# Performance work log

Hardware: AMD Instinct MI355X
Metric: run time of the kernel (lower is better)

## Reference

```python
import jax, jax.numpy as jnp
import numpy as np

# Sobel kernels stacked as [O=2, I=1, 3, 3]
_KX = np.array([[-1., 0., 1.], [-2., 0., 2.], [-1., 0., 1.]], dtype=np.float32)
_KY = np.array([[1., 2., 1.], [0., 0., 0.], [-1., -2., -1.]], dtype=np.float32)
_SOBEL_W = jnp.asarray(np.stack([_KX, _KY])[:, None, :, :])  # [2,1,3,3]


def _sobel(x):
    # x: [B,1,H,W] -> |Gx| + |Gy| : [B,1,H,W]
    g = jax.lax.conv_general_dilated(
        x, _SOBEL_W, window_strides=(1, 1), padding=((1, 1), (1, 1)),
        dimension_numbers=('NCHW', 'OIHW', 'NCHW'))  # [B,2,H,W]
    return jnp.sum(jnp.abs(g), axis=1, keepdims=True)


def _threshold_mask(g, k):
    # g: [B,1,H,W]; k-th SMALLEST over flattened (C*H*W) per batch (torch.kthvalue)
    B, N, H, W = g.shape
    flat = g.reshape(B, N, H * W)
    kth = jnp.sort(flat, axis=-1)[:, :, k - 1:k]  # [B,N,1]
    mask = (flat >= kth).astype(g.dtype)
    return mask.reshape(B, N, H, W)


def setup_inputs() -> dict:
    key = jax.random.key(0)
    kA, kB, kF = jax.random.split(key, 3)
    shape = (8, 3, 1024, 1024)
    return {
        'image_A': jax.random.uniform(kA, shape, dtype=jnp.float32),
        'image_B': jax.random.uniform(kB, shape, dtype=jnp.float32),
        'image_fused': jax.random.uniform(kF, shape, dtype=jnp.float32),
        'thresholds': 524288,
    }


def reference(image_A, image_B, image_fused, thresholds):
    gA = _sobel(image_A[:, :1])
    gB = _sobel(image_B[:, :1])
    gF = _sobel(image_fused[:, :1])
    joint_max = jnp.maximum(gA, gB)  # max over concat([gA,gB], dim=1) with 1 ch each
    maskA = _threshold_mask(gA, thresholds)
    maskB = _threshold_mask(gB, thresholds)
    loss = jnp.mean(jnp.abs(gF - joint_max))
    return (loss, maskA, maskB)
```

## Files before the change

### kernel.cpp

```cpp
#include <hip/hip_runtime.h>

#define IMG_H 1024
#define IMG_W 1024
#define NBATCH 8
#define NCH 3
#define NPIX (IMG_H * IMG_W)
#define SEGS 64
#define NTOT (8388608LL)

#define BINS1 4096
#define SH1 19

#define WS_MISC_OFF   0
#define WS_MISC_BYTES 4096
#define WS_H1R_OFF    (WS_MISC_OFF + WS_MISC_BYTES)
#define WS_H1R_BYTES  (2 * NBATCH * BINS1 * 4)
#define WS_H1P_OFF    (WS_H1R_OFF + WS_H1R_BYTES)
#define WS_H1P_BYTES  (2 * NBATCH * SEGS * BINS1 * 2)
#define WS_LIST_OFF   (WS_H1P_OFF + WS_H1P_BYTES)

struct Row3f { float l, c, r; };

__device__ __forceinline__ Row3f load3(const float* __restrict__ img, int y, int x) {
    Row3f o;
    if ((unsigned)y >= (unsigned)IMG_H) { o.l = o.c = o.r = 0.0f; return o; }
    const float* row = img + (size_t)y * IMG_W;
    o.c = row[x];
    o.l = (x > 0)         ? row[x - 1] : 0.0f;
    o.r = (x < IMG_W - 1) ? row[x + 1] : 0.0f;
    return o;
}

__device__ __forceinline__ float sobel_g(const Row3f& r0, const Row3f& r1, const Row3f& r2) {
    float gx = r0.r - r0.l;
    gx -= 2.0f * r1.l;
    gx += 2.0f * r1.r;
    gx -= r2.l;
    gx += r2.r;
    float gy = r0.l + 2.0f * r0.c;
    gy += r0.r;
    gy -= r2.l;
    gy -= 2.0f * r2.c;
    gy -= r2.r;
    return fabsf(gx) + fabsf(gy);
}

extern "C" __global__ __launch_bounds__(512)
void k_pass0(const float* __restrict__ A, const float* __restrict__ B,
             const float* __restrict__ F,
             unsigned short* __restrict__ hist1p, double* __restrict__ lossAcc)
{
    __shared__ unsigned int h[4 * BINS1];
    __shared__ double lsum[8];
    const int t = threadIdx.x;
    for (int i = t; i < 4 * BINS1; i += 512) h[i] = 0u;
    __syncthreads();

    const int blk = blockIdx.x;
    const int batch = blk >> 6;
    const int seg = blk & 63;
    const int y0 = (seg >> 1) * 32;
    const int x  = (seg & 1) * 512 + t;
    unsigned int* hc = h + (t >> 8) * (2 * BINS1);

    const float* a = A + (size_t)batch * NCH * NPIX;
    const float* b = B + (size_t)batch * NCH * NPIX;
    const float* f = F + (size_t)batch * NCH * NPIX;

    Row3f a0 = load3(a, y0 - 1, x), a1 = load3(a, y0, x), a2;
    Row3f b0 = load3(b, y0 - 1, x), b1 = load3(b, y0, x), b2;
    Row3f f0 = load3(f, y0 - 1, x), f1 = load3(f, y0, x), f2;

    double loss = 0.0;
    for (int i = 0; i < 32; ++i) {
        const int y = y0 + i;
        a2 = load3(a, y + 1, x);
        b2 = load3(b, y + 1, x);
        f2 = load3(f, y + 1, x);
        const float gA = sobel_g(a0, a1, a2);
        const float gB = sobel_g(b0, b1, b2);
        const float gF = sobel_g(f0, f1, f2);
        atomicAdd(&hc[__float_as_uint(gA) >> SH1], 1u);
        atomicAdd(&hc[BINS1 + (__float_as_uint(gB) >> SH1)], 1u);
        loss += (double)fabsf(gF - fmaxf(gA, gB));
        a0 = a1; a1 = a2;
        b0 = b1; b1 = b2;
        f0 = f1; f1 = f2;
    }
    __syncthreads();

    unsigned short* oA = hist1p + ((size_t)batch            * SEGS + seg) * BINS1;
    unsigned short* oB = hist1p + ((size_t)(NBATCH + batch) * SEGS + seg) * BINS1;
    for (int i = t; i < 2 * BINS1; i += 512) {
        const unsigned v = h[i] + h[2 * BINS1 + i];
        if (i < BINS1) oA[i] = (unsigned short)v;
        else           oB[i - BINS1] = (unsigned short)v;
    }

    for (int off = 32; off > 0; off >>= 1) loss += __shfl_down(loss, off);
    if ((t & 63) == 0) lsum[t >> 6] = loss;
    __syncthreads();
    if (t == 0) {
        double s = 0.0;
        for (int i = 0; i < 8; ++i) s += lsum[i];
        atomicAdd(lossAcc, s);
    }
}

extern "C" __global__ __launch_bounds__(256)
void k_scan1a(const unsigned short* __restrict__ hist1p, unsigned int* __restrict__ hist1r)
{
    const int idx = blockIdx.x * 256 + threadIdx.x;
    const int ib  = idx >> 12;
    const int bin = idx & (BINS1 - 1);
    const unsigned short* p = hist1p + (size_t)ib * SEGS * BINS1 + bin;
    unsigned int s = 0;
    #pragma unroll 8
    for (int sg = 0; sg < SEGS; ++sg) s += p[(size_t)sg * BINS1];
    hist1r[idx] = s;
}

extern "C" __global__ __launch_bounds__(1024)
void k_scan1b(const unsigned int* __restrict__ hist1r, const int* __restrict__ kptr,
              int* __restrict__ sel1, int* __restrict__ resid1)
{
    const int ib = blockIdx.x, t = threadIdx.x;
    const unsigned int* hr = hist1r + (size_t)ib * BINS1;
    long long kl = (long long)kptr[0];
    if (kl < 1 || kl > (long long)NPIX) {
        float kf = ((const float*)kptr)[0];
        kl = (long long)kf;
        if (kl < 1) kl = 1;
        if (kl > NPIX) kl = NPIX;
    }
    const unsigned k = (unsigned)kl;

    const uint4 c = ((const uint4*)hr)[t];
    const unsigned s = c.x + c.y + c.z + c.w;
    __shared__ unsigned ls[1024];
    ls[t] = s; __syncthreads();
    for (int off = 1; off < 1024; off <<= 1) {
        unsigned v = (t >= off) ? ls[t - off] : 0u;
        __syncthreads();
        ls[t] += v;
        __syncthreads();
    }
    const unsigned incl = ls[t];
    const unsigned excl = incl - s;
    if (excl < k && k <= incl) {
        unsigned cum = excl; int bin = t * 4;
        if (cum + c.x < k) { cum += c.x; ++bin;
          if (cum + c.y < k) { cum += c.y; ++bin;
            if (cum + c.z < k) { cum += c.z; ++bin; } } }
        sel1[ib] = bin;
        resid1[ib] = (int)(k - cum);
    }
}

#define PB_ROWS 32
extern "C" __global__ __launch_bounds__(1024)
void k_passB(const float* __restrict__ A, const float* __restrict__ B,
             const int* __restrict__ sel1, unsigned int* __restrict__ gCnt,
             uint2* __restrict__ list, unsigned cap, float* __restrict__ out)
{
    const int t = threadIdx.x;
    const int blk = blockIdx.x;
    const int batch = blk >> 5;
    const int y0 = (blk & 31) * PB_ROWS;
    const int x = t;

    const float* a = A + (size_t)batch * NCH * NPIX;
    const float* b = B + (size_t)batch * NCH * NPIX;
    const unsigned sA = (unsigned)sel1[batch];
    const unsigned sB = (unsigned)sel1[NBATCH + batch];
    float* mA = out + 1 + (size_t)batch * NPIX;
    float* mB = out + 1 + (size_t)NTOT + (size_t)batch * NPIX;

    __shared__ uint2 bufA[2048], bufB[2048];
    __shared__ unsigned cntA, cntB, baseA, baseB;
    if (t == 0) { cntA = 0u; cntB = 0u; }
    __syncthreads();

    Row3f a0 = load3(a, y0 - 1, x), a1 = load3(a, y0, x), a2;
    Row3f b0 = load3(b, y0 - 1, x), b1 = load3(b, y0, x), b2;
    for (int i = 0; i < PB_ROWS; ++i) {
        const int y = y0 + i;
        a2 = load3(a, y + 1, x);
        b2 = load3(b, y + 1, x);
        const unsigned uA = __float_as_uint(sobel_g(a0, a1, a2));
        const unsigned uB = __float_as_uint(sobel_g(b0, b1, b2));
        const unsigned binA = uA >> SH1, binB = uB >> SH1;
        const unsigned idx = (unsigned)y * IMG_W + (unsigned)x;
        mA[idx] = (binA > sA) ? 1.0f : 0.0f;
        mB[idx] = (binB > sB) ? 1.0f : 0.0f;
        if (binA == sA) { unsigned p = atomicAdd(&cntA, 1u); bufA[p] = make_uint2(uA, idx); }
        if (binB == sB) { unsigned p = atomicAdd(&cntB, 1u); bufB[p] = make_uint2(uB, idx); }
        a0 = a1; a1 = a2;
        b0 = b1; b1 = b2;

        __syncthreads();
        const bool last = (i == PB_ROWS - 1);
        const unsigned nA = cntA, nB = cntB;
        const bool doA = (nA >= 1024u) || (last && nA > 0u);
        const bool doB = (nB >= 1024u) || (last && nB > 0u);
        if (doA || doB) {
            if (t == 0) {
                if (doA) baseA = atomicAdd(&gCnt[batch], nA);
                if (doB) baseB = atomicAdd(&gCnt[NBATCH + batch], nB);
            }
            __syncthreads();
            if (doA) {
                const unsigned bs = baseA;
                for (unsigned j = t; j < nA; j += 1024u) {
                    const unsigned d = bs + j;
                    if (d < cap) list[(size_t)batch * cap + d] = bufA[j];
                }
            }
            if (doB) {
                const unsigned bs = baseB;
                for (unsigned j = t; j < nB; j += 1024u) {
                    const unsigned d = bs + j;
                    if (d < cap) list[(size_t)(NBATCH + batch) * cap + d] = bufB[j];
                }
            }
            __syncthreads();
            if (t == 0) { if (doA) cntA = 0u; if (doB) cntB = 0u; }
        }
        __syncthreads();
    }
}

extern "C" __global__ __launch_bounds__(1024)
void k_selectfix(const uint2* __restrict__ list, const unsigned int* __restrict__ gCnt,
                 unsigned cap, const int* __restrict__ sel1, const int* __restrict__ resid1,
                 const double* __restrict__ lossAcc, float* __restrict__ out)
{
    const int ib = blockIdx.x, t = threadIdx.x;
    const unsigned n = min(gCnt[ib], cap);
    const unsigned kk = (unsigned)resid1[ib];
    const uint2* L = list + (size_t)ib * cap;

    __shared__ unsigned h2[BINS1];
    __shared__ unsigned ls[1024];
    __shared__ unsigned bcast[4];
    if (t < 4) bcast[t] = 0u;
    for (int i = t; i < BINS1; i += 1024) h2[i] = 0u;
    __syncthreads();

    for (unsigned j = t; j < n; j += 1024u) atomicAdd(&h2[(L[j].x >> 7) & 4095u], 1u);
    __syncthreads();

    const unsigned c0 = h2[4 * t], c1 = h2[4 * t + 1], c2 = h2[4 * t + 2], c3 = h2[4 * t + 3];
    const unsigned s = c0 + c1 + c2 + c3;
    ls[t] = s; __syncthreads();
    for (int off = 1; off < 1024; off <<= 1) {
        unsigned v = (t >= off) ? ls[t - off] : 0u;
        __syncthreads();
        ls[t] += v;
        __syncthreads();
    }
    {
        const unsigned incl = ls[t], excl = incl - s;
        if (excl < kk && kk <= incl) {
            unsigned cum = excl; unsigned bin = 4u * t;
            if (cum + c0 < kk) { cum += c0; ++bin;
              if (cum + c1 < kk) { cum += c1; ++bin;
                if (cum + c2 < kk) { cum += c2; ++bin; } } }
            bcast[0] = bin;
            bcast[1] = kk - cum;
        }
    }
    __syncthreads();
    const unsigned sel2 = bcast[0], k3 = bcast[1];

    if (t < 128) h2[t] = 0u;
    __syncthreads();
    for (unsigned j = t; j < n; j += 1024u) {
        const unsigned b = L[j].x;
        if (((b >> 7) & 4095u) == sel2) atomicAdd(&h2[b & 127u], 1u);
    }
    __syncthreads();
    {
        const unsigned s3 = (t < 128) ? h2[t] : 0u;
        ls[t] = s3; __syncthreads();
        for (int off = 1; off < 1024; off <<= 1) {
            unsigned v = (t >= off) ? ls[t - off] : 0u;
            __syncthreads();
            ls[t] += v;
            __syncthreads();
        }
        const unsigned incl = ls[t], excl = incl - s3;
        if (t < 128 && excl < k3 && k3 <= incl) {
            bcast[2] = ((unsigned)sel1[ib] << SH1) | (sel2 << 7) | (unsigned)t;
        }
    }
    __syncthreads();
    const unsigned kth = bcast[2];

    float* m = out + 1 + (size_t)ib * NPIX;
    for (unsigned j = t; j < n; j += 1024u) {
        const uint2 e = L[j];
        m[e.y] = (e.x >= kth) ? 1.0f : 0.0f;
    }
    if (ib == 0 && t == 0) out[0] = (float)(lossAcc[0] * (1.0 / 8388608.0));
}

extern "C" void kernel_launch(void* const* d_in, const int* in_sizes, int n_in,
                              void* d_out, int out_size, void* d_ws, size_t ws_size,
                              hipStream_t stream)
{
    const float* A = (const float*)d_in[0];
    const float* B = (const float*)d_in[1];
    const float* F = (const float*)d_in[2];
    const int* kptr = (const int*)d_in[3];
    float* out = (float*)d_out;

    if (ws_size < (size_t)WS_LIST_OFF + 16 * 8 * 1024) return;

    char* ws = (char*)d_ws;
    double* lossAcc        = (double*)(ws + WS_MISC_OFF);
    unsigned int* gCnt     = (unsigned int*)(ws + WS_MISC_OFF + 64);
    unsigned int* hist1r   = (unsigned int*)(ws + WS_H1R_OFF);
    unsigned short* hist1p = (unsigned short*)(ws + WS_H1P_OFF);
    uint2* list            = (uint2*)(ws + WS_LIST_OFF);
    int* sel1              = (int*)(ws + WS_MISC_OFF + 128);
    int* resid1            = (int*)(ws + WS_MISC_OFF + 256);

    unsigned long long capll = (ws_size - WS_LIST_OFF) / (16ull * 8ull);
    unsigned cap = (capll > (unsigned long long)NPIX) ? (unsigned)NPIX : (unsigned)capll;

    hipMemsetAsync(ws, 0, WS_MISC_BYTES, stream);

    k_pass0    <<<dim3(NBATCH * SEGS), dim3(512), 0, stream>>>(A, B, F, hist1p, lossAcc);
    k_scan1a   <<<dim3(2 * NBATCH * BINS1 / 256), dim3(256), 0, stream>>>(hist1p, hist1r);
    k_scan1b   <<<dim3(2 * NBATCH), dim3(1024), 0, stream>>>(hist1r, kptr, sel1, resid1);
    k_passB    <<<dim3(NBATCH * 32), dim3(1024), 0, stream>>>(A, B, sel1, gCnt, list, cap, out);
    k_selectfix<<<dim3(2 * NBATCH), dim3(1024), 0, stream>>>(list, gCnt, cap, sel1, resid1, lossAcc, out);
}
```

Before: 346.9 us.

## Merge histogram via global atomics, drop scan kernel, use wave-shuffle scans

Per-block histograms are now added directly into the global reduced histogram with atomics on nonzero bins. This removes the 16-bit partial-histogram buffer and the separate reduction kernel. The loss is written as per-block partials and summed inside the new select kernel, which also resets the list counters so the misc memset can go. Block-wide prefix scans are replaced by wave shuffle scans plus a small cross-wave pass, cutting barrier count. Pass0 and passB now use 1024 threads with 16-row segments, doubling passB's grid, at the cost of global atomic contention on the shared histogram.

Measured after the change: 322.5 us. -7.0%, faster.

```diff
diff --git a/kernel.cpp b/kernel.cpp
--- a/kernel.cpp
+++ b/kernel.cpp
@@ -5,19 +5,20 @@
 #define NBATCH 8
 #define NCH 3
 #define NPIX (IMG_H * IMG_W)
-#define SEGS 64
 #define NTOT (8388608LL)
 
 #define BINS1 4096
 #define SH1 19
 
+#define SEGS 64
+#define ROWS_PER_SEG 16
+
 #define WS_MISC_OFF   0
-#define WS_MISC_BYTES 4096
-#define WS_H1R_OFF    (WS_MISC_OFF + WS_MISC_BYTES)
+#define WS_H1R_OFF    4096
 #define WS_H1R_BYTES  (2 * NBATCH * BINS1 * 4)
-#define WS_H1P_OFF    (WS_H1R_OFF + WS_H1R_BYTES)
-#define WS_H1P_BYTES  (2 * NBATCH * SEGS * BINS1 * 2)
-#define WS_LIST_OFF   (WS_H1P_OFF + WS_H1P_BYTES)
+#define WS_LOSSP_OFF  (WS_H1R_OFF + WS_H1R_BYTES)
+#define WS_LOSSP_BYTES (NBATCH * SEGS * 8)
+#define WS_LIST_OFF   (WS_LOSSP_OFF + WS_LOSSP_BYTES)
 
 struct Row3f { float l, c, r; };
 
@@ -45,23 +46,32 @@
     return fabsf(gx) + fabsf(gy);
 }
 
-extern "C" __global__ __launch_bounds__(512)
+__device__ __forceinline__ unsigned wave_scan(unsigned s, int lane) {
+    #pragma unroll
+    for (int off = 1; off < 64; off <<= 1) {
+        const unsigned v = __shfl_up(s, off);
+        if (lane >= off) s += v;
+    }
+    return s;
+}
+
+extern "C" __global__ __launch_bounds__(1024)
 void k_pass0(const float* __restrict__ A, const float* __restrict__ B,
              const float* __restrict__ F,
-             unsigned short* __restrict__ hist1p, double* __restrict__ lossAcc)
+             unsigned int* __restrict__ hist1r, double* __restrict__ lossPart)
 {
     __shared__ unsigned int h[4 * BINS1];
-    __shared__ double lsum[8];
+    __shared__ double lsum[16];
     const int t = threadIdx.x;
-    for (int i = t; i < 4 * BINS1; i += 512) h[i] = 0u;
+    const int lane = t & 63;
+    for (int i = t; i < 4 * BINS1; i += 1024) h[i] = 0u;
     __syncthreads();
 
     const int blk = blockIdx.x;
     const int batch = blk >> 6;
-    const int seg = blk & 63;
-    const int y0 = (seg >> 1) * 32;
-    const int x  = (seg & 1) * 512 + t;
-    unsigned int* hc = h + (t >> 8) * (2 * BINS1);
+    const int y0 = (blk & 63) * ROWS_PER_SEG;
+    const int x = t;
+    unsigned int* hc = h + (t >> 9) * (2 * BINS1);
 
     const float* a = A + (size_t)batch * NCH * NPIX;
     const float* b = B + (size_t)batch * NCH * NPIX;
@@ -72,7 +82,7 @@
     Row3f f0 = load3(f, y0 - 1, x), f1 = load3(f, y0, x), f2;
 
     double loss = 0.0;
-    for (int i = 0; i < 32; ++i) {
+    for (int i = 0; i < ROWS_PER_SEG; ++i) {
         const int y = y0 + i;
         a2 = load3(a, y + 1, x);
         b2 = load3(b, y + 1, x);
@@ -89,43 +99,34 @@
     }
     __syncthreads();
 
-    unsigned short* oA = hist1p + ((size_t)batch            * SEGS + seg) * BINS1;
-    unsigned short* oB = hist1p + ((size_t)(NBATCH + batch) * SEGS + seg) * BINS1;
-    for (int i = t; i < 2 * BINS1; i += 512) {
+    for (int i = t; i < 2 * BINS1; i += 1024) {
         const unsigned v = h[i] + h[2 * BINS1 + i];
-        if (i < BINS1) oA[i] = (unsigned short)v;
-        else           oB[i - BINS1] = (unsigned short)v;
+        if (v) {
+            unsigned int* dst = (i < BINS1)
+                ? &hist1r[(size_t)batch * BINS1 + i]
+                : &hist1r[(size_t)(NBATCH + batch) * BINS1 + (i - BINS1)];
+            atomicAdd(dst, v);
+        }
     }
 
     for (int off = 32; off > 0; off >>= 1) loss += __shfl_down(loss, off);
-    if ((t & 63) == 0) lsum[t >> 6] = loss;
+    if (lane == 0) lsum[t >> 6] = loss;
     __syncthreads();
     if (t == 0) {
         double s = 0.0;
-        for (int i = 0; i < 8; ++i) s += lsum[i];
-        atomicAdd(lossAcc, s);
-    }
-}
-
-extern "C" __global__ __launch_bounds__(256)
-void k_scan1a(const unsigned short* __restrict__ hist1p, unsigned int* __restrict__ hist1r)
-{
-    const int idx = blockIdx.x * 256 + threadIdx.x;
-    const int ib  = idx >> 12;
-    const int bin = idx & (BINS1 - 1);
-    const unsigned short* p = hist1p + (size_t)ib * SEGS * BINS1 + bin;
-    unsigned int s = 0;
-    #pragma unroll 8
-    for (int sg = 0; sg < SEGS; ++sg) s += p[(size_t)sg * BINS1];
-    hist1r[idx] = s;
+        for (int i = 0; i < 16; ++i) s += lsum[i];
+        lossPart[blk] = s;
+    }
 }
 
 extern "C" __global__ __launch_bounds__(1024)
-void k_scan1b(const unsigned int* __restrict__ hist1r, const int* __restrict__ kptr,
-              int* __restrict__ sel1, int* __restrict__ resid1)
+void k_select1(const unsigned int* __restrict__ hist1r, const double* __restrict__ lossPart,
+               const int* __restrict__ kptr, int* __restrict__ sel1, int* __restrict__ resid1,
+               double* __restrict__ lossAcc, unsigned int* __restrict__ gCnt)
 {
     const int ib = blockIdx.x, t = threadIdx.x;
-    const unsigned int* hr = hist1r + (size_t)ib * BINS1;
+    const int lane = t & 63, wid = t >> 6;
+
     long long kl = (long long)kptr[0];
     if (kl < 1 || kl > (long long)NPIX) {
         float kf = ((const float*)kptr)[0];
@@ -135,17 +136,22 @@
     }
     const unsigned k = (unsigned)kl;
 
-    const uint4 c = ((const uint4*)hr)[t];
+    const uint4 c = ((const uint4*)(hist1r + (size_t)ib * BINS1))[t];
     const unsigned s = c.x + c.y + c.z + c.w;
-    __shared__ unsigned ls[1024];
-    ls[t] = s; __syncthreads();
-    for (int off = 1; off < 1024; off <<= 1) {
-        unsigned v = (t >= off) ? ls[t - off] : 0u;
-        __syncthreads();
-        ls[t] += v;
-        __syncthreads();
-    }
-    const unsigned incl = ls[t];
+
+    unsigned incl = wave_scan(s, lane);
+    __shared__ unsigned wsum[16];
+    __shared__ double dsum[16];
+    if (lane == 63) wsum[wid] = incl;
+    __syncthreads();
+    if (wid == 0) {
+        unsigned w = (lane < 16) ? wsum[lane] : 0u;
+        w = wave_scan(w, lane);
+        if (lane < 16) wsum[lane] = w;
+    }
+    __syncthreads();
+    if (wid > 0) incl += wsum[wid - 1];
+
     const unsigned excl = incl - s;
     if (excl < k && k <= incl) {
         unsigned cum = excl; int bin = t * 4;
@@ -155,9 +161,20 @@
         sel1[ib] = bin;
         resid1[ib] = (int)(k - cum);
     }
-}
-
-#define PB_ROWS 32
+
+    double v = 0.0;
+    if (ib == 0 && t < NBATCH * SEGS) v = lossPart[t];
+    for (int off = 32; off > 0; off >>= 1) v += __shfl_down(v, off);
+    if (lane == 0) dsum[wid] = v;
+    __syncthreads();
+    if (ib == 0 && t == 0) {
+        double sL = 0.0;
+        for (int i = 0; i < 16; ++i) sL += dsum[i];
+        lossAcc[0] = sL;
+    }
+    if (t == 0) gCnt[ib] = 0u;
+}
+
 extern "C" __global__ __launch_bounds__(1024)
 void k_passB(const float* __restrict__ A, const float* __restrict__ B,
              const int* __restrict__ sel1, unsigned int* __restrict__ gCnt,
@@ -165,8 +182,8 @@
 {
     const int t = threadIdx.x;
     const int blk = blockIdx.x;
-    const int batch = blk >> 5;
-    const int y0 = (blk & 31) * PB_ROWS;
+    const int batch = blk >> 6;
+    const int y0 = (blk & 63) * ROWS_PER_SEG;
     const int x = t;
 
     const float* a = A + (size_t)batch * NCH * NPIX;
@@ -183,7 +200,7 @@
 
     Row3f a0 = load3(a, y0 - 1, x), a1 = load3(a, y0, x), a2;
     Row3f b0 = load3(b, y0 - 1, x), b1 = load3(b, y0, x), b2;
-    for (int i = 0; i < PB_ROWS; ++i) {
+    for (int i = 0; i < ROWS_PER_SEG; ++i) {
         const int y = y0 + i;
         a2 = load3(a, y + 1, x);
         b2 = load3(b, y + 1, x);
@@ -199,7 +216,7 @@
         b0 = b1; b1 = b2;
 
         __syncthreads();
-        const bool last = (i == PB_ROWS - 1);
+        const bool last = (i == ROWS_PER_SEG - 1);
         const unsigned nA = cntA, nB = cntB;
         const bool doA = (nA >= 1024u) || (last && nA > 0u);
         const bool doB = (nB >= 1024u) || (last && nB > 0u);
@@ -236,12 +253,13 @@
                  const double* __restrict__ lossAcc, float* __restrict__ out)
 {
     const int ib = blockIdx.x, t = threadIdx.x;
-    const unsigned n = min(gCnt[ib], cap);
+    const int lane = t & 63, wid = t >> 6;
+    unsigned n = gCnt[ib]; if (n > cap) n = cap;
     const unsigned kk = (unsigned)resid1[ib];
     const uint2* L = list + (size_t)ib * cap;
 
     __shared__ unsigned h2[BINS1];
-    __shared__ unsigned ls[1024];
+    __shared__ unsigned wsum[16];
     __shared__ unsigned bcast[4];
     if (t < 4) bcast[t] = 0u;
     for (int i = t; i < BINS1; i += 1024) h2[i] = 0u;
@@ -252,15 +270,18 @@
 
     const unsigned c0 = h2[4 * t], c1 = h2[4 * t + 1], c2 = h2[4 * t + 2], c3 = h2[4 * t + 3];
     const unsigned s = c0 + c1 + c2 + c3;
-    ls[t] = s; __syncthreads();
-    for (int off = 1; off < 1024; off <<= 1) {
-        unsigned v = (t >= off) ? ls[t - off] : 0u;
-        __syncthreads();
-        ls[t] += v;
-        __syncthreads();
-    }
+    unsigned incl = wave_scan(s, lane);
+    if (lane == 63) wsum[wid] = incl;
+    __syncthreads();
+    if (wid == 0) {
+        unsigned w = (lane < 16) ? wsum[lane] : 0u;
+        w = wave_scan(w, lane);
+        if (lane < 16) wsum[lane] = w;
+    }
+    __syncthreads();
+    if (wid > 0) incl += wsum[wid - 1];
     {
-        const unsigned incl = ls[t], excl = incl - s;
+        const unsigned excl = incl - s;
         if (excl < kk && kk <= incl) {
             unsigned cum = excl; unsigned bin = 4u * t;
             if (cum + c0 < kk) { cum += c0; ++bin;
@@ -276,21 +297,24 @@
     if (t < 128) h2[t] = 0u;
     __syncthreads();
     for (unsigned j = t; j < n; j += 1024u) {
-        const unsigned b = L[j].x;
-        if (((b >> 7) & 4095u) == sel2) atomicAdd(&h2[b & 127u], 1u);
+        const unsigned bbits = L[j].x;
+        if (((bbits >> 7) & 4095u) == sel2) atomicAdd(&h2[bbits & 127u], 1u);
     }
     __syncthreads();
     {
         const unsigned s3 = (t < 128) ? h2[t] : 0u;
-        ls[t] = s3; __syncthreads();
-        for (int off = 1; off < 1024; off <<= 1) {
-            unsigned v = (t >= off) ? ls[t - off] : 0u;
-            __syncthreads();
-            ls[t] += v;
-            __syncthreads();
-        }
-        const unsigned incl = ls[t], excl = incl - s3;
-        if (t < 128 && excl < k3 && k3 <= incl) {
+        unsigned incl3 = wave_scan(s3, lane);
+        if (lane == 63) wsum[wid] = incl3;
+        __syncthreads();
+        if (wid == 0) {
+            unsigned w = (lane < 16) ? wsum[lane] : 0u;
+            w = wave_scan(w, lane);
+            if (lane < 16) wsum[lane] = w;
+        }
+        __syncthreads();
+        if (wid > 0) incl3 += wsum[wid - 1];
+        const unsigned excl3 = incl3 - s3;
+        if (t < 128 && excl3 < k3 && k3 <= incl3) {
             bcast[2] = ((unsigned)sel1[ib] << SH1) | (sel2 << 7) | (unsigned)t;
         }
     }
@@ -320,20 +344,19 @@
     char* ws = (char*)d_ws;
     double* lossAcc        = (double*)(ws + WS_MISC_OFF);
     unsigned int* gCnt     = (unsigned int*)(ws + WS_MISC_OFF + 64);
-    unsigned int* hist1r   = (unsigned int*)(ws + WS_H1R_OFF);
-    unsigned short* hist1p = (unsigned short*)(ws + WS_H1P_OFF);
-    uint2* list            = (uint2*)(ws + WS_LIST_OFF);
     int* sel1              = (int*)(ws + WS_MISC_OFF + 128);
     int* resid1            = (int*)(ws + WS_MISC_OFF + 256);
+    unsigned int* hist1r   = (unsigned int*)(ws + WS_H1R_OFF);
+    double* lossPart       = (double*)(ws + WS_LOSSP_OFF);
+    uint2* list            = (uint2*)(ws + WS_LIST_OFF);
 
     unsigned long long capll = (ws_size - WS_LIST_OFF) / (16ull * 8ull);
     unsigned cap = (capll > (unsigned long long)NPIX) ? (unsigned)NPIX : (unsigned)capll;
 
-    hipMemsetAsync(ws, 0, WS_MISC_BYTES, stream);
-
-    k_pass0    <<<dim3(NBATCH * SEGS), dim3(512), 0, stream>>>(A, B, F, hist1p, lossAcc);
-    k_scan1a   <<<dim3(2 * NBATCH * BINS1 / 256), dim3(256), 0, stream>>>(hist1p, hist1r);
-    k_scan1b   <<<dim3(2 * NBATCH), dim3(1024), 0, stream>>>(hist1r, kptr, sel1, resid1);
-    k_passB    <<<dim3(NBATCH * 32), dim3(1024), 0, stream>>>(A, B, sel1, gCnt, list, cap, out);
+    hipMemsetAsync(ws + WS_H1R_OFF, 0, WS_H1R_BYTES, stream);
+
+    k_pass0    <<<dim3(NBATCH * SEGS), dim3(1024), 0, stream>>>(A, B, F, hist1r, lossPart);
+    k_select1  <<<dim3(2 * NBATCH), dim3(1024), 0, stream>>>(hist1r, lossPart, kptr, sel1, resid1, lossAcc, gCnt);
+    k_passB    <<<dim3(NBATCH * SEGS), dim3(1024), 0, stream>>>(A, B, sel1, gCnt, list, cap, out);
     k_selectfix<<<dim3(2 * NBATCH), dim3(1024), 0, stream>>>(list, gCnt, cap, sel1, resid1, lossAcc, out);
 }
```
